# Kernel tuning notes

Measured on AMD Instinct MI355X. Metric: run time of the kernel, lower is better.

Reference implementation:

```python
import jax, jax.numpy as jnp
import numpy as np

EMB = 2048; H = 32; G = 8; D = 64; GS = H // G; EPS = 1e-6

def _rmsnorm(x, scale):
    x32 = x.astype(jnp.float32)
    var = jnp.mean(x32 * x32, axis=-1, keepdims=True)
    return (x32 * jax.lax.rsqrt(var + EPS) * scale).astype(x.dtype)

def _rope(x, cos, sin):
    # x: [B, h, S, D]; cos/sin: [S, D]
    d = x.shape[-1]
    x1, x2 = x[..., : d // 2], x[..., d // 2 :]
    rot = jnp.concatenate([-x2, x1], axis=-1)
    return (x * cos[None, None] + rot * sin[None, None]).astype(x.dtype)

def setup_inputs() -> dict:
    key = jax.random.key(0)
    ks = jax.random.split(key, 6)
    B, S = 2, 2048
    x = jax.random.normal(ks[0], (B, S, EMB), jnp.float32)
    # causal mask: True = blocked (masked_fill semantics)
    mask = jnp.triu(jnp.ones((S, S), dtype=bool), k=1)
    # standard RoPE tables, half-dim rotation, shape [S, D]
    inv_freq = 1.0 / (10000.0 ** (jnp.arange(0, D, 2, dtype=jnp.float32) / D))
    ang = jnp.arange(S, dtype=jnp.float32)[:, None] * inv_freq[None, :]  # [S, D/2]
    cos = jnp.concatenate([jnp.cos(ang), jnp.cos(ang)], axis=-1)
    sin = jnp.concatenate([jnp.sin(ang), jnp.sin(ang)], axis=-1)
    Wq = jax.random.normal(ks[1], (EMB, H * D), jnp.float32) * 0.02
    Wk = jax.random.normal(ks[2], (EMB, G * D), jnp.float32) * 0.02
    Wv = jax.random.normal(ks[3], (EMB, G * D), jnp.float32) * 0.02
    Wo = jax.random.normal(ks[4], (H * D, EMB), jnp.float32) * 0.02
    q_scale = jnp.ones((D,), jnp.float32)
    k_scale = jnp.ones((D,), jnp.float32)
    return {"x": x, "mask": mask, "cos": cos, "sin": sin, "Wq": Wq, "Wk": Wk,
            "Wv": Wv, "Wo": Wo, "q_scale": q_scale, "k_scale": k_scale}

def reference(x, mask, cos, sin, Wq, Wk, Wv, Wo, q_scale, k_scale):
    B, S, _ = x.shape
    q = (x @ Wq).reshape(B, S, H, D).transpose(0, 2, 1, 3)  # [B,H,S,D]
    k = (x @ Wk).reshape(B, S, G, D).transpose(0, 2, 1, 3)  # [B,G,S,D]
    v = (x @ Wv).reshape(B, S, G, D).transpose(0, 2, 1, 3)
    q = _rmsnorm(q, q_scale)
    k = _rmsnorm(k, k_scale)
    q = _rope(q, cos, sin)
    k = _rope(k, cos, sin)
    # GQA expansion (repeat_interleave over head dim)
    k = jnp.repeat(k, GS, axis=1)
    v = jnp.repeat(v, GS, axis=1)
    scale = 1.0 / np.float32(np.sqrt(D))
    s = jnp.einsum('bhqd,bhkd->bhqk', q.astype(jnp.float32), k.astype(jnp.float32)) * scale
    # flash path is causal regardless of `mask` arg; mask here equals causal
    s = jnp.where(mask[None, None], -jnp.inf, s)
    w = jax.nn.softmax(s, axis=-1)
    ctx = jnp.einsum('bhqk,bhkd->bhqd', w, v.astype(jnp.float32))
    ctx = ctx.transpose(0, 2, 1, 3).reshape(B, S, H * D)
    return ctx @ Wo
```

## Files before the change

### kernel.cpp

```cpp
#include <hip/hip_runtime.h>
#include <hip/hip_bf16.h>
#include <cstdint>
#include <cstddef>

#define EMB   2048
#define NH_   32
#define NG_   8
#define DH_   64
#define SEQ_  2048
#define BB_   2
#define MTOT  4096
#define LDQKV 3072
#define SM_C  0.18033688f

typedef __attribute__((ext_vector_type(8))) short s16x8;
typedef __attribute__((ext_vector_type(8))) unsigned short u16x8;
typedef __attribute__((ext_vector_type(4))) float f32x4;
typedef __attribute__((ext_vector_type(16))) float f32x16;
typedef __attribute__((ext_vector_type(4))) unsigned int u32x4;
typedef __attribute__((ext_vector_type(2))) unsigned int u32x2;
typedef __attribute__((ext_vector_type(2))) int i32x2;

__device__ __forceinline__ float bf2f(unsigned short u) {
  unsigned int x = (unsigned int)u << 16; return __uint_as_float(x);
}
__device__ __forceinline__ unsigned short f2bf(float f) {
  unsigned int x = __float_as_uint(f);
  x = x + 0x7FFFu + ((x >> 16) & 1u);
  return (unsigned short)(x >> 16);
}
__device__ __forceinline__ float ninf() { return __int_as_float(0xff800000); }
__device__ __forceinline__ unsigned int pack_bf2(float a, float b) {
  unsigned int r;
  asm("v_cvt_pk_bf16_f32 %0, %1, %2" : "=v"(r) : "v"(a), "v"(b));
  return r;
}
__device__ __forceinline__ void plswap(unsigned int& a, unsigned int& b) {
  i32x2 r = __builtin_amdgcn_permlane32_swap((int)a, (int)b, false, false);
  a = (unsigned int)r[0]; b = (unsigned int)r[1];
}
__device__ __forceinline__ void plswapf(float& a, float& b) {
  unsigned int ua = __float_as_uint(a), ub = __float_as_uint(b);
  plswap(ua, ub);
  a = __uint_as_float(ua); b = __uint_as_float(ub);
}

__device__ __forceinline__ void glds16(const void* g, void* l) {
  __builtin_amdgcn_global_load_lds((const __attribute__((address_space(1))) void*)g,
                                   (__attribute__((address_space(3))) void*)l, 16, 0, 0);
}

__device__ __forceinline__ void hw_sincos(float ang, float& c, float& s) {
  float rev = ang * 0.15915494309f;
  rev = rev - floorf(rev);
  asm("v_cos_f32 %0, %1" : "=v"(c) : "v"(rev));
  asm("v_sin_f32 %0, %1" : "=v"(s) : "v"(rev));
}

__global__ __launch_bounds__(256)
void prep(const float* __restrict__ x, const float* __restrict__ Wq,
          const float* __restrict__ Wk, const float* __restrict__ Wv,
          const float* __restrict__ Wo, unsigned short* __restrict__ xb,
          unsigned short* __restrict__ Wt, unsigned short* __restrict__ Wot) {
  __shared__ float tile[64][65];
  const int tid = threadIdx.x;
  const int bid = blockIdx.x;
  if (bid < 4096) {
    size_t i = (size_t)bid * 256 + tid;
    float4 a = *(const float4*)(x + i * 8);
    float4 c = *(const float4*)(x + i * 8 + 4);
    u16x8 o;
    o[0] = f2bf(a.x); o[1] = f2bf(a.y); o[2] = f2bf(a.z); o[3] = f2bf(a.w);
    o[4] = f2bf(c.x); o[5] = f2bf(c.y); o[6] = f2bf(c.z); o[7] = f2bf(c.w);
    *(u16x8*)(xb + i * 8) = o;
    return;
  }
  const float* in; unsigned short* out; int N; int local;
  if (bid < 5120)      { in = Wq; out = Wt;                       N = 2048; local = bid - 4096; }
  else if (bid < 5376) { in = Wk; out = Wt + (size_t)2048 * 2048; N = 512;  local = bid - 5120; }
  else if (bid < 5632) { in = Wv; out = Wt + (size_t)2560 * 2048; N = 512;  local = bid - 5376; }
  else                 { in = Wo; out = Wot;                      N = 2048; local = bid - 5632; }
  const int ntile = N >> 6;
  const int n0 = (local % ntile) * 64, k0 = (local / ntile) * 64;
  #pragma unroll
  for (int jj = 0; jj < 4; ++jj) {
    int r = (tid >> 4) + jj * 16;
    int c = (tid & 15) * 4;
    float4 v = *(const float4*)(in + (size_t)(k0 + r) * N + n0 + c);
    tile[r][c] = v.x; tile[r][c + 1] = v.y; tile[r][c + 2] = v.z; tile[r][c + 3] = v.w;
  }
  __syncthreads();
  #pragma unroll
  for (int rep = 0; rep < 2; ++rep) {
    int u = rep * 256 + tid;
    int nl = u >> 3, ch = u & 7;
    u16x8 o;
    #pragma unroll
    for (int e = 0; e < 8; ++e) o[e] = f2bf(tile[ch * 8 + e][nl]);
    *(u16x8*)(out + (size_t)(n0 + nl) * 2048 + k0 + ch * 8) = o;
  }
}

template<int BN, int F32OUT>
__global__ __launch_bounds__(512, 1)
void gemm256(const unsigned short* __restrict__ A, const unsigned short* __restrict__ Bt,
             void* __restrict__ C, int ldc) {
  constexpr int NST = 2 + BN / 128;
  constexpr int BUF = 16384 + BN * 64;
  constexpr int WN = BN / 64;
  constexpr int RW = 256 / (8 / WN);
  __shared__ __align__(16) char L[4][BUF];
  const int tid = threadIdx.x;
  const int wid = tid >> 6, lane = tid & 63;
  const int wm = wid / WN, wn = wid % WN;
  const int grp = lane >> 4, l15 = lane & 15;
  const int bm = blockIdx.y * 256, bn = blockIdx.x * BN;
  const int nt = 64;

  const int srow = tid >> 2;
  const int sc = (tid & 3) ^ (srow & 3);
  const int grp2 = grp ^ (l15 & 3);

  auto stage_ht = [&](int t, int h) {
    const unsigned short* src = (h < 2)
      ? A  + (size_t)(bm + h * 128 + srow) * 2048 + t * 32 + sc * 8
      : Bt + (size_t)(bn + (h - 2) * 128 + srow) * 2048 + t * 32 + sc * 8;
    glds16(src, &L[t & 3][h * 8192 + wid * 1024]);
  };

  f32x4 acc[RW / 16][4] = {};

  #pragma unroll
  for (int h = 0; h < NST; ++h) stage_ht(0, h);
  #pragma unroll
  for (int h = 0; h < NST; ++h) stage_ht(1, h);
  if constexpr (BN == 256) asm volatile("s_waitcnt vmcnt(4)" ::: "memory");
  else                     asm volatile("s_waitcnt vmcnt(3)" ::: "memory");
  __builtin_amdgcn_sched_barrier(0);
  __builtin_amdgcn_s_barrier();
  __builtin_amdgcn_sched_barrier(0);

  for (int t = 0; t < nt; ++t) {
    const char* Ab = &L[t & 3][0]     + (size_t)(wm * RW + l15) * 64 + grp2 * 16;
    const char* Bb = &L[t & 3][16384] + (size_t)(wn * 64 + l15) * 64 + grp2 * 16;
    const bool pre = (t + 2 < nt);
    if (pre) { stage_ht(t + 2, 0); stage_ht(t + 2, 1); }
    s16x8 bf[4], af[4];
    #pragma unroll
    for (int j = 0; j < 4; ++j) bf[j] = *(const s16x8*)(Bb + j * 1024);
    #pragma unroll
    for (int i = 0; i < 4; ++i) af[i] = *(const s16x8*)(Ab + i * 1024);
    __builtin_amdgcn_s_setprio(1);
    #pragma unroll
    for (int i = 0; i < 4; ++i)
      #pragma unroll
      for (int j = 0; j < 4; ++j)
        acc[i][j] = __builtin_amdgcn_mfma_f32_16x16x32_bf16(af[i], bf[j], acc[i][j], 0, 0, 0);
    __builtin_amdgcn_s_setprio(0);
    if constexpr (BN == 256) {
      if (pre) { stage_ht(t + 2, 2); stage_ht(t + 2, 3); }
      #pragma unroll
      for (int i = 0; i < 4; ++i) af[i] = *(const s16x8*)(Ab + (4 + i) * 1024);
      __builtin_amdgcn_s_setprio(1);
      #pragma unroll
      for (int i = 0; i < 4; ++i)
        #pragma unroll
        for (int j = 0; j < 4; ++j)
          acc[4 + i][j] = __builtin_amdgcn_mfma_f32_16x16x32_bf16(af[i], bf[j], acc[4 + i][j], 0, 0, 0);
      __builtin_amdgcn_s_setprio(0);
    } else {
      if (pre) stage_ht(t + 2, 2);
    }
    if (t + 1 < nt) {
      if (pre) {
        if constexpr (BN == 256) asm volatile("s_waitcnt vmcnt(4)" ::: "memory");
        else                     asm volatile("s_waitcnt vmcnt(3)" ::: "memory");
      } else {
        asm volatile("s_waitcnt vmcnt(0)" ::: "memory");
      }
      __builtin_amdgcn_sched_barrier(0);
      __builtin_amdgcn_s_barrier();
      __builtin_amdgcn_sched_barrier(0);
    }
  }

  #pragma unroll
  for (int i = 0; i < RW / 16; ++i)
    #pragma unroll
    for (int j = 0; j < 4; ++j)
      #pragma unroll
      for (int r = 0; r < 4; ++r) {
        int row = bm + wm * RW + i * 16 + grp * 4 + r;
        int col = bn + wn * 64 + j * 16 + l15;
        float v = acc[i][j][r];
        if (F32OUT) ((float*)C)[(size_t)row * ldc + col] = v;
        else        ((unsigned short*)C)[(size_t)row * ldc + col] = f2bf(v);
      }
}

__global__ __launch_bounds__(256)
void kvtile_rms(const unsigned short* __restrict__ qkv, const float* __restrict__ ksc,
                const float* __restrict__ cs, const float* __restrict__ sn,
                unsigned short* __restrict__ Kt, unsigned short* __restrict__ Vt) {
  __shared__ unsigned short Kl[32][72];
  __shared__ unsigned short Vl[32][72];
  const int tid = threadIdx.x;
  const int kt = blockIdx.x;
  const int bg = blockIdx.y;
  const int b = bg >> 3, g = bg & 7;
  {
    const int row = tid >> 3, ch = tid & 7;
    const int spos = kt * 32 + row;
    u16x8 kv = *(const u16x8*)(qkv + (size_t)(b * SEQ_ + spos) * LDQKV + 2048 + g * 64 + ch * 8);
    float v[8]; float sq = 0.f;
    #pragma unroll
    for (int e = 0; e < 8; ++e) { v[e] = bf2f(kv[e]); sq += v[e] * v[e]; }
    sq += __shfl_xor(sq, 1); sq += __shfl_xor(sq, 2); sq += __shfl_xor(sq, 4);
    const float rn = rsqrtf(sq * (1.f / 64.f) + 1e-6f);
    float xn[8];
    #pragma unroll
    for (int e = 0; e < 8; ++e) xn[e] = v[e] * rn * ksc[ch * 8 + e];
    float pn[8];
    #pragma unroll
    for (int e = 0; e < 8; ++e) pn[e] = __shfl_xor(xn[e], 4);
    const bool lo = (ch < 4);
    #pragma unroll
    for (int e = 0; e < 8; ++e) {
      int d = ch * 8 + e;
      float c = cs[spos * 64 + d], si = sn[spos * 64 + d];
      float o = lo ? (xn[e] * c - pn[e] * si) : fmaf(xn[e], c, pn[e] * si);
      Kl[row][d] = f2bf(o);
    }
    u16x8 vv = *(const u16x8*)(qkv + (size_t)(b * SEQ_ + spos) * LDQKV + 2560 + g * 64 + ch * 8);
    #pragma unroll
    for (int e = 0; e < 8; ++e) Vl[row][ch * 8 + e] = vv[e];
  }
  __syncthreads();
  {
    int c = tid >> 5, row = tid & 31;
    u16x8 o;
    #pragma unroll
    for (int e = 0; e < 8; ++e) o[e] = Kl[row][c * 8 + e];
    *(u16x8*)(Kt + (((size_t)(bg * 64 + kt)) << 11) + (c * 32 + row) * 8) = o;
  }
  {
    int c = tid >> 6, d = tid & 63;
    u16x8 o;
    #pragma unroll
    for (int e = 0; e < 8; ++e) o[e] = Vl[c * 8 + e][d];
    *(u16x8*)(Vt + (((size_t)(bg * 64 + kt)) << 11) + (c * 64 + d) * 8) = o;
  }
}

__global__ __launch_bounds__(256)
void attn_mfma11(const unsigned short* __restrict__ qkv, const float* __restrict__ qsc,
                 const unsigned short* __restrict__ Ktg, const unsigned short* __restrict__ Vtg,
                 unsigned short* __restrict__ ctx) {
  __shared__ __align__(16) unsigned short LA[8 * 1024];
  __shared__ __align__(16) unsigned short LB[8 * 1024];
  const int tid = threadIdx.x;
  const int w = tid >> 6, lane = tid & 63;
  const int l31 = lane & 31, half = lane >> 5;
  const int bid = blockIdx.x;
  const int x8 = bid & 7, r = bid >> 3;
  const int bg = x8 + 8 * (r & 1);
  const int rr = r >> 1;
  const int slot = rr >> 4, gi = rr & 15;
  const int qt = (slot == 0) ? (63 - gi) : (slot == 1) ? gi
               : (slot == 2) ? (47 - gi) : (16 + gi);
  const int b = bg >> 3, g = bg & 7, h = g * 4 + w;
  const int qbase = qt * 32;
  const int nkt = qt + 1;
  const int nit = (nkt + 1) >> 1;

  s16x8 qf[4];
  {
    const int spos = qbase + l31;
    float qv[4][8]; float sq = 0.f;
    #pragma unroll
    for (int s = 0; s < 4; ++s) {
      u16x8 raw = *(const u16x8*)(qkv + (size_t)(b * SEQ_ + spos) * LDQKV + h * 64 + half * 8 + s * 16);
      #pragma unroll
      for (int e = 0; e < 8; ++e) { qv[s][e] = bf2f(raw[e]); sq += qv[s][e] * qv[s][e]; }
    }
    sq += __shfl_xor(sq, 32);
    const float rn = rsqrtf(sq * (1.f / 64.f) + 1e-6f);
    float xn[4][8];
    #pragma unroll
    for (int s = 0; s < 4; ++s)
      #pragma unroll
      for (int e = 0; e < 8; ++e) xn[s][e] = qv[s][e] * rn * qsc[s * 16 + half * 8 + e];
    const float fs = (float)spos;
    float qo[4][8];
    #pragma unroll
    for (int s = 0; s < 2; ++s)
      #pragma unroll
      for (int e = 0; e < 8; ++e) {
        int d = s * 16 + half * 8 + e;
        float invf = exp2f((float)d * -0.4152410119f);
        float c0, s0;
        hw_sincos(fs * invf, c0, s0);
        qo[s][e]     = (xn[s][e] * c0 - xn[s + 2][e] * s0) * SM_C;
        qo[s + 2][e] = fmaf(xn[s + 2][e], c0, xn[s][e] * s0) * SM_C;
      }
    #pragma unroll
    for (int s = 0; s < 4; ++s) {
      u32x4 t;
      t[0] = pack_bf2(qo[s][0], qo[s][1]); t[1] = pack_bf2(qo[s][2], qo[s][3]);
      t[2] = pack_bf2(qo[s][4], qo[s][5]); t[3] = pack_bf2(qo[s][6], qo[s][7]);
      qf[s] = __builtin_bit_cast(s16x8, t);
    }
  }

  f32x16 acc0 = {}, acc1 = {};
  float l_st = 0.f;

  const size_t tbase = ((size_t)(bg * 64)) << 11;
  const int soff = (w << 9) + lane * 8;

  auto stage = [&](unsigned short* Lb, int pi) {
    const int kt0 = 2 * pi, kt1 = 2 * pi + 1;
    glds16(Ktg + tbase + ((size_t)kt0 << 11) + soff, (char*)Lb + (w << 10));
    glds16(Vtg + tbase + ((size_t)kt0 << 11) + soff, (char*)Lb + 8192 + (w << 10));
    if (kt1 < nkt) {
      glds16(Ktg + tbase + ((size_t)kt1 << 11) + soff, (char*)Lb + 4096 + (w << 10));
      glds16(Vtg + tbase + ((size_t)kt1 << 11) + soff, (char*)Lb + 12288 + (w << 10));
    }
  };

  auto sub = [&](const char* Kb, const char* Vb, bool diag, float& lsum) {
    s16x8 KF0 = *(const s16x8*)(Kb + (((0 + half) << 5) + l31) * 16);
    s16x8 KF1 = *(const s16x8*)(Kb + (((2 + half) << 5) + l31) * 16);
    s16x8 KF2 = *(const s16x8*)(Kb + (((4 + half) << 5) + l31) * 16);
    s16x8 KF3 = *(const s16x8*)(Kb + (((6 + half) << 5) + l31) * 16);
    s16x8 vf00 = *(const s16x8*)(Vb + (((half) << 6) + l31) * 16);
    s16x8 vf01 = *(const s16x8*)(Vb + (((2 + half) << 6) + l31) * 16);
    s16x8 vf10 = *(const s16x8*)(Vb + (((half) << 6) + 32 + l31) * 16);
    s16x8 vf11 = *(const s16x8*)(Vb + (((2 + half) << 6) + 32 + l31) * 16);
    f32x16 st = {};
    __builtin_amdgcn_s_setprio(1);
    st = __builtin_amdgcn_mfma_f32_32x32x16_bf16(KF0, qf[0], st, 0, 0, 0);
    st = __builtin_amdgcn_mfma_f32_32x32x16_bf16(KF1, qf[1], st, 0, 0, 0);
    st = __builtin_amdgcn_mfma_f32_32x32x16_bf16(KF2, qf[2], st, 0, 0, 0);
    st = __builtin_amdgcn_mfma_f32_32x32x16_bf16(KF3, qf[3], st, 0, 0, 0);
    __builtin_amdgcn_s_setprio(0);
    if (diag) {
      #pragma unroll
      for (int r2 = 0; r2 < 16; ++r2) {
        int key = (r2 & 3) + 8 * (r2 >> 2) + 4 * half;
        if (key > l31) st[r2] = ninf();
      }
    }
    float p[16];
    #pragma unroll
    for (int r2 = 0; r2 < 16; ++r2) p[r2] = exp2f(st[r2]);
    float s8[8];
    #pragma unroll
    for (int r2 = 0; r2 < 8; ++r2) s8[r2] = p[r2] + p[r2 + 8];
    lsum += ((s8[0] + s8[1]) + (s8[2] + s8[3])) + ((s8[4] + s8[5]) + (s8[6] + s8[7]));
    unsigned int PK[8];
    #pragma unroll
    for (int j = 0; j < 8; ++j) PK[j] = pack_bf2(p[2 * j], p[2 * j + 1]);
    plswap(PK[0], PK[2]); plswap(PK[1], PK[3]);
    plswap(PK[4], PK[6]); plswap(PK[5], PK[7]);
    u32x4 pb0u, pb1u;
    pb0u[0] = PK[0]; pb0u[1] = PK[1]; pb0u[2] = PK[2]; pb0u[3] = PK[3];
    pb1u[0] = PK[4]; pb1u[1] = PK[5]; pb1u[2] = PK[6]; pb1u[3] = PK[7];
    s16x8 pb0 = __builtin_bit_cast(s16x8, pb0u);
    s16x8 pb1 = __builtin_bit_cast(s16x8, pb1u);
    __builtin_amdgcn_s_setprio(1);
    acc0 = __builtin_amdgcn_mfma_f32_32x32x16_bf16(vf00, pb0, acc0, 0, 0, 0);
    acc1 = __builtin_amdgcn_mfma_f32_32x32x16_bf16(vf10, pb0, acc1, 0, 0, 0);
    acc0 = __builtin_amdgcn_mfma_f32_32x32x16_bf16(vf01, pb1, acc0, 0, 0, 0);
    acc1 = __builtin_amdgcn_mfma_f32_32x32x16_bf16(vf11, pb1, acc1, 0, 0, 0);
    __builtin_amdgcn_s_setprio(0);
  };

  auto pair_body = [&](const unsigned short* Lb, int pi) {
    const int kt0 = 2 * pi, kt1 = 2 * pi + 1;
    float lsum = 0.f;
    sub((const char*)Lb, (const char*)Lb + 8192, kt0 == qt, lsum);
    if (kt1 < nkt)
      sub((const char*)Lb + 4096, (const char*)Lb + 12288, kt1 == qt, lsum);
    { float a2 = lsum, b2 = lsum; plswapf(a2, b2); lsum = a2 + b2; }
    l_st += lsum;
  };

  stage(LA, 0);
  int pi = 0;
  while (true) {
    __syncthreads();
    if (pi + 1 < nit) stage(LB, pi + 1);
    pair_body(LA, pi);
    ++pi; if (pi >= nit) break;
    __syncthreads();
    if (pi + 1 < nit) stage(LA, pi + 1);
    pair_body(LB, pi);
    ++pi; if (pi >= nit) break;
  }

  const float linv = 1.f / l_st;
  unsigned short* orow = ctx + (size_t)(b * SEQ_ + qbase + l31) * 2048 + h * 64;
  #pragma unroll
  for (int dt = 0; dt < 2; ++dt) {
    #pragma unroll
    for (int rq = 0; rq < 4; ++rq) {
      const int rr2 = rq * 4;
      const int d0 = dt * 32 + 8 * rq + 4 * half;
      float a0 = (dt ? acc1[rr2]     : acc0[rr2])     * linv;
      float a1 = (dt ? acc1[rr2 + 1] : acc0[rr2 + 1]) * linv;
      float a2 = (dt ? acc1[rr2 + 2] : acc0[rr2 + 2]) * linv;
      float a3 = (dt ? acc1[rr2 + 3] : acc0[rr2 + 3]) * linv;
      u32x2 o;
      o[0] = pack_bf2(a0, a1);
      o[1] = pack_bf2(a2, a3);
      *(u32x2*)(orow + d0) = o;
    }
  }
}

extern "C" void kernel_launch(void* const* d_in, const int* in_sizes, int n_in,
                              void* d_out, int out_size, void* d_ws, size_t ws_size,
                              hipStream_t stream) {
  const float* x  = (const float*)d_in[0];
  const float* cs = (const float*)d_in[2];
  const float* sn = (const float*)d_in[3];
  const float* Wq = (const float*)d_in[4];
  const float* Wk = (const float*)d_in[5];
  const float* Wv = (const float*)d_in[6];
  const float* Wo = (const float*)d_in[7];
  const float* qs = (const float*)d_in[8];
  const float* ks = (const float*)d_in[9];
  float* out = (float*)d_out;

  unsigned short* xb  = (unsigned short*)d_ws;
  unsigned short* Wt  = xb  + (size_t)4096 * 2048;
  unsigned short* Wot = Wt  + (size_t)3072 * 2048;
  unsigned short* qkv = Wot + (size_t)2048 * 2048;
  unsigned short* vTb = qkv + (size_t)4096 * 3072;
  unsigned short* ctx = vTb + (size_t)16 * 64 * 2048;
  unsigned short* Ktt = xb;

  prep<<<6656, 256, 0, stream>>>(x, Wq, Wk, Wv, Wo, xb, Wt, Wot);
  gemm256<256, 0><<<dim3(12, 16), 512, 0, stream>>>(xb, Wt, qkv, 3072);
  kvtile_rms<<<dim3(64, 16), 256, 0, stream>>>(qkv, ks, cs, sn, Ktt, vTb);
  attn_mfma11<<<1024, 256, 0, stream>>>(qkv, qs, Ktt, vTb, ctx);
  gemm256<128, 1><<<dim3(16, 16), 512, 0, stream>>>(ctx, Wot, out, 2048);
}
```

Measured before the change: 184.4 us.

## Split long causal query tiles across blocks and merge partials in a combine kernel

Causal attention work is rebalanced so every block does a near-equal amount of key tiles. Long query tiles (32-63) are split at key tile 32. The first half runs alone in one block and the second half is paired with a short query tile (31-j) in another block. Unnormalized partial outputs and row sums go to reused workspace buffers, and a new combine kernel adds the two partials and normalizes them. The GEMM LDS swizzle pattern is also changed to XOR with (row>>1)&3. The split adds an extra launch, partial-buffer traffic and a second bf16 rounding of the partials, in exchange for removing the tail imbalance.

```diff
diff --git a/kernel.cpp b/kernel.cpp
--- a/kernel.cpp
+++ b/kernel.cpp
@@ -118,8 +118,8 @@
   const int nt = 64;
 
   const int srow = tid >> 2;
-  const int sc = (tid & 3) ^ (srow & 3);
-  const int grp2 = grp ^ (l15 & 3);
+  const int sc = (tid & 3) ^ ((srow >> 1) & 3);
+  const int grp2 = grp ^ ((l15 >> 1) & 3);
 
   auto stage_ht = [&](int t, int h) {
     const unsigned short* src = (h < 2)
@@ -253,170 +253,223 @@
 }
 
 __global__ __launch_bounds__(256)
-void attn_mfma11(const unsigned short* __restrict__ qkv, const float* __restrict__ qsc,
+void attn_mfma12(const unsigned short* __restrict__ qkv, const float* __restrict__ qsc,
                  const unsigned short* __restrict__ Ktg, const unsigned short* __restrict__ Vtg,
-                 unsigned short* __restrict__ ctx) {
-  __shared__ __align__(16) unsigned short LA[8 * 1024];
-  __shared__ __align__(16) unsigned short LB[8 * 1024];
+                 unsigned short* __restrict__ xbt, unsigned short* __restrict__ WtS,
+                 float* __restrict__ lbuf, unsigned short* __restrict__ ctx) {
+  __shared__ __align__(16) unsigned short LA[10 * 1024];
+  __shared__ __align__(16) unsigned short LB[10 * 1024];
   const int tid = threadIdx.x;
   const int w = tid >> 6, lane = tid & 63;
   const int l31 = lane & 31, half = lane >> 5;
   const int bid = blockIdx.x;
-  const int x8 = bid & 7, r = bid >> 3;
-  const int bg = x8 + 8 * (r & 1);
-  const int rr = r >> 1;
-  const int slot = rr >> 4, gi = rr & 15;
-  const int qt = (slot == 0) ? (63 - gi) : (slot == 1) ? gi
-               : (slot == 2) ? (47 - gi) : (16 + gi);
+  const int x8 = bid & 7, c = bid >> 3;
+  const int bg = x8 + 8 * (c & 1);
+  const int c2 = c >> 1;
   const int b = bg >> 3, g = bg & 7, h = g * 4 + w;
-  const int qbase = qt * 32;
-  const int nkt = qt + 1;
-  const int nit = (nkt + 1) >> 1;
-
-  s16x8 qf[4];
-  {
-    const int spos = qbase + l31;
-    float qv[4][8]; float sq = 0.f;
-    #pragma unroll
-    for (int s = 0; s < 4; ++s) {
-      u16x8 raw = *(const u16x8*)(qkv + (size_t)(b * SEQ_ + spos) * LDQKV + h * 64 + half * 8 + s * 16);
-      #pragma unroll
-      for (int e = 0; e < 8; ++e) { qv[s][e] = bf2f(raw[e]); sq += qv[s][e] * qv[s][e]; }
-    }
-    sq += __shfl_xor(sq, 32);
-    const float rn = rsqrtf(sq * (1.f / 64.f) + 1e-6f);
-    float xn[4][8];
-    #pragma unroll
-    for (int s = 0; s < 4; ++s)
-      #pragma unroll
-      for (int e = 0; e < 8; ++e) xn[s][e] = qv[s][e] * rn * qsc[s * 16 + half * 8 + e];
-    const float fs = (float)spos;
-    float qo[4][8];
-    #pragma unroll
-    for (int s = 0; s < 2; ++s)
-      #pragma unroll
-      for (int e = 0; e < 8; ++e) {
-        int d = s * 16 + half * 8 + e;
-        float invf = exp2f((float)d * -0.4152410119f);
-        float c0, s0;
-        hw_sincos(fs * invf, c0, s0);
-        qo[s][e]     = (xn[s][e] * c0 - xn[s + 2][e] * s0) * SM_C;
-        qo[s + 2][e] = fmaf(xn[s + 2][e], c0, xn[s][e] * s0) * SM_C;
-      }
-    #pragma unroll
-    for (int s = 0; s < 4; ++s) {
-      u32x4 t;
-      t[0] = pack_bf2(qo[s][0], qo[s][1]); t[1] = pack_bf2(qo[s][2], qo[s][3]);
-      t[2] = pack_bf2(qo[s][4], qo[s][5]); t[3] = pack_bf2(qo[s][6], qo[s][7]);
-      qf[s] = __builtin_bit_cast(s16x8, t);
-    }
-  }
-
-  f32x16 acc0 = {}, acc1 = {};
-  float l_st = 0.f;
+
+  int nseg, sqt[2], sk0[2], slen[2], smode[2], sslot[2];
+  if (c2 < 32) {
+    nseg = 1;
+    sqt[0] = 32 + c2; sk0[0] = 0; slen[0] = 32; smode[0] = 1;
+    sslot[0] = ((bg * 4 + w) * 32 + c2) * 2 + 0;
+  } else {
+    const int j = c2 - 32;
+    nseg = 2;
+    sqt[0] = 32 + j;  sk0[0] = 32; slen[0] = j + 1;  smode[0] = 1;
+    sslot[0] = ((bg * 4 + w) * 32 + j) * 2 + 1;
+    sqt[1] = 31 - j;  sk0[1] = 0;  slen[1] = 32 - j; smode[1] = 0; sslot[1] = 0;
+  }
 
   const size_t tbase = ((size_t)(bg * 64)) << 11;
   const int soff = (w << 9) + lane * 8;
 
-  auto stage = [&](unsigned short* Lb, int pi) {
-    const int kt0 = 2 * pi, kt1 = 2 * pi + 1;
-    glds16(Ktg + tbase + ((size_t)kt0 << 11) + soff, (char*)Lb + (w << 10));
-    glds16(Vtg + tbase + ((size_t)kt0 << 11) + soff, (char*)Lb + 8192 + (w << 10));
-    if (kt1 < nkt) {
-      glds16(Ktg + tbase + ((size_t)kt1 << 11) + soff, (char*)Lb + 4096 + (w << 10));
-      glds16(Vtg + tbase + ((size_t)kt1 << 11) + soff, (char*)Lb + 12288 + (w << 10));
-    }
-  };
-
-  auto sub = [&](const char* Kb, const char* Vb, bool diag, float& lsum) {
-    s16x8 KF0 = *(const s16x8*)(Kb + (((0 + half) << 5) + l31) * 16);
-    s16x8 KF1 = *(const s16x8*)(Kb + (((2 + half) << 5) + l31) * 16);
-    s16x8 KF2 = *(const s16x8*)(Kb + (((4 + half) << 5) + l31) * 16);
-    s16x8 KF3 = *(const s16x8*)(Kb + (((6 + half) << 5) + l31) * 16);
-    s16x8 vf00 = *(const s16x8*)(Vb + (((half) << 6) + l31) * 16);
-    s16x8 vf01 = *(const s16x8*)(Vb + (((2 + half) << 6) + l31) * 16);
-    s16x8 vf10 = *(const s16x8*)(Vb + (((half) << 6) + 32 + l31) * 16);
-    s16x8 vf11 = *(const s16x8*)(Vb + (((2 + half) << 6) + 32 + l31) * 16);
-    f32x16 st = {};
-    __builtin_amdgcn_s_setprio(1);
-    st = __builtin_amdgcn_mfma_f32_32x32x16_bf16(KF0, qf[0], st, 0, 0, 0);
-    st = __builtin_amdgcn_mfma_f32_32x32x16_bf16(KF1, qf[1], st, 0, 0, 0);
-    st = __builtin_amdgcn_mfma_f32_32x32x16_bf16(KF2, qf[2], st, 0, 0, 0);
-    st = __builtin_amdgcn_mfma_f32_32x32x16_bf16(KF3, qf[3], st, 0, 0, 0);
-    __builtin_amdgcn_s_setprio(0);
-    if (diag) {
-      #pragma unroll
-      for (int r2 = 0; r2 < 16; ++r2) {
-        int key = (r2 & 3) + 8 * (r2 >> 2) + 4 * half;
-        if (key > l31) st[r2] = ninf();
+  for (int s = 0; s < nseg; ++s) {
+    const int qt = sqt[s], k0 = sk0[s];
+    const int kend = k0 + slen[s];
+    const int qbase = qt * 32;
+
+    s16x8 qf[4];
+    {
+      const int spos = qbase + l31;
+      float qv[4][8]; float sq = 0.f;
+      #pragma unroll
+      for (int s2 = 0; s2 < 4; ++s2) {
+        u16x8 raw = *(const u16x8*)(qkv + (size_t)(b * SEQ_ + spos) * LDQKV + h * 64 + half * 8 + s2 * 16);
+        #pragma unroll
+        for (int e = 0; e < 8; ++e) { qv[s2][e] = bf2f(raw[e]); sq += qv[s2][e] * qv[s2][e]; }
+      }
+      sq += __shfl_xor(sq, 32);
+      const float rn = rsqrtf(sq * (1.f / 64.f) + 1e-6f);
+      float xn[4][8];
+      #pragma unroll
+      for (int s2 = 0; s2 < 4; ++s2)
+        #pragma unroll
+        for (int e = 0; e < 8; ++e) xn[s2][e] = qv[s2][e] * rn * qsc[s2 * 16 + half * 8 + e];
+      const float fs = (float)spos;
+      float qo[4][8];
+      #pragma unroll
+      for (int s2 = 0; s2 < 2; ++s2)
+        #pragma unroll
+        for (int e = 0; e < 8; ++e) {
+          int d = s2 * 16 + half * 8 + e;
+          float invf = exp2f((float)d * -0.4152410119f);
+          float c0, s0;
+          hw_sincos(fs * invf, c0, s0);
+          qo[s2][e]     = (xn[s2][e] * c0 - xn[s2 + 2][e] * s0) * SM_C;
+          qo[s2 + 2][e] = fmaf(xn[s2 + 2][e], c0, xn[s2][e] * s0) * SM_C;
+        }
+      #pragma unroll
+      for (int s2 = 0; s2 < 4; ++s2) {
+        u32x4 t;
+        t[0] = pack_bf2(qo[s2][0], qo[s2][1]); t[1] = pack_bf2(qo[s2][2], qo[s2][3]);
+        t[2] = pack_bf2(qo[s2][4], qo[s2][5]); t[3] = pack_bf2(qo[s2][6], qo[s2][7]);
+        qf[s2] = __builtin_bit_cast(s16x8, t);
       }
     }
-    float p[16];
-    #pragma unroll
-    for (int r2 = 0; r2 < 16; ++r2) p[r2] = exp2f(st[r2]);
-    float s8[8];
-    #pragma unroll
-    for (int r2 = 0; r2 < 8; ++r2) s8[r2] = p[r2] + p[r2 + 8];
-    lsum += ((s8[0] + s8[1]) + (s8[2] + s8[3])) + ((s8[4] + s8[5]) + (s8[6] + s8[7]));
-    unsigned int PK[8];
-    #pragma unroll
-    for (int j = 0; j < 8; ++j) PK[j] = pack_bf2(p[2 * j], p[2 * j + 1]);
-    plswap(PK[0], PK[2]); plswap(PK[1], PK[3]);
-    plswap(PK[4], PK[6]); plswap(PK[5], PK[7]);
-    u32x4 pb0u, pb1u;
-    pb0u[0] = PK[0]; pb0u[1] = PK[1]; pb0u[2] = PK[2]; pb0u[3] = PK[3];
-    pb1u[0] = PK[4]; pb1u[1] = PK[5]; pb1u[2] = PK[6]; pb1u[3] = PK[7];
-    s16x8 pb0 = __builtin_bit_cast(s16x8, pb0u);
-    s16x8 pb1 = __builtin_bit_cast(s16x8, pb1u);
-    __builtin_amdgcn_s_setprio(1);
-    acc0 = __builtin_amdgcn_mfma_f32_32x32x16_bf16(vf00, pb0, acc0, 0, 0, 0);
-    acc1 = __builtin_amdgcn_mfma_f32_32x32x16_bf16(vf10, pb0, acc1, 0, 0, 0);
-    acc0 = __builtin_amdgcn_mfma_f32_32x32x16_bf16(vf01, pb1, acc0, 0, 0, 0);
-    acc1 = __builtin_amdgcn_mfma_f32_32x32x16_bf16(vf11, pb1, acc1, 0, 0, 0);
-    __builtin_amdgcn_s_setprio(0);
-  };
-
-  auto pair_body = [&](const unsigned short* Lb, int pi) {
-    const int kt0 = 2 * pi, kt1 = 2 * pi + 1;
-    float lsum = 0.f;
-    sub((const char*)Lb, (const char*)Lb + 8192, kt0 == qt, lsum);
-    if (kt1 < nkt)
-      sub((const char*)Lb + 4096, (const char*)Lb + 12288, kt1 == qt, lsum);
-    { float a2 = lsum, b2 = lsum; plswapf(a2, b2); lsum = a2 + b2; }
-    l_st += lsum;
-  };
-
-  stage(LA, 0);
-  int pi = 0;
-  while (true) {
+
+    f32x16 acc0 = {}, acc1 = {};
+    float l_st = 0.f;
+
+    auto stage = [&](unsigned short* Lb, int ktA) {
+      glds16(Ktg + tbase + ((size_t)ktA << 11) + soff, (char*)Lb + (w << 10));
+      glds16(Vtg + tbase + ((size_t)ktA << 11) + soff, (char*)Lb + 8192 + (w << 10));
+      if (ktA + 1 < kend) {
+        glds16(Ktg + tbase + ((size_t)(ktA + 1) << 11) + soff, (char*)Lb + 4096 + (w << 10));
+        glds16(Vtg + tbase + ((size_t)(ktA + 1) << 11) + soff, (char*)Lb + 12288 + (w << 10));
+      }
+    };
+
+    auto sub = [&](const char* Kb, const char* Vb, bool diag, float& lsum) {
+      s16x8 KF0 = *(const s16x8*)(Kb + (((0 + half) << 5) + l31) * 16);
+      s16x8 KF1 = *(const s16x8*)(Kb + (((2 + half) << 5) + l31) * 16);
+      s16x8 KF2 = *(const s16x8*)(Kb + (((4 + half) << 5) + l31) * 16);
+      s16x8 KF3 = *(const s16x8*)(Kb + (((6 + half) << 5) + l31) * 16);
+      s16x8 vf00 = *(const s16x8*)(Vb + (((half) << 6) + l31) * 16);
+      s16x8 vf01 = *(const s16x8*)(Vb + (((2 + half) << 6) + l31) * 16);
+      s16x8 vf10 = *(const s16x8*)(Vb + (((half) << 6) + 32 + l31) * 16);
+      s16x8 vf11 = *(const s16x8*)(Vb + (((2 + half) << 6) + 32 + l31) * 16);
+      f32x16 st = {};
+      __builtin_amdgcn_s_setprio(1);
+      st = __builtin_amdgcn_mfma_f32_32x32x16_bf16(KF0, qf[0], st, 0, 0, 0);
+      st = __builtin_amdgcn_mfma_f32_32x32x16_bf16(KF1, qf[1], st, 0, 0, 0);
+      st = __builtin_amdgcn_mfma_f32_32x32x16_bf16(KF2, qf[2], st, 0, 0, 0);
+      st = __builtin_amdgcn_mfma_f32_32x32x16_bf16(KF3, qf[3], st, 0, 0, 0);
+      __builtin_amdgcn_s_setprio(0);
+      if (diag) {
+        #pragma unroll
+        for (int r2 = 0; r2 < 16; ++r2) {
+          int key = (r2 & 3) + 8 * (r2 >> 2) + 4 * half;
+          if (key > l31) st[r2] = ninf();
+        }
+      }
+      float p[16];
+      #pragma unroll
+      for (int r2 = 0; r2 < 16; ++r2) p[r2] = exp2f(st[r2]);
+      float s8[8];
+      #pragma unroll
+      for (int r2 = 0; r2 < 8; ++r2) s8[r2] = p[r2] + p[r2 + 8];
+      lsum += ((s8[0] + s8[1]) + (s8[2] + s8[3])) + ((s8[4] + s8[5]) + (s8[6] + s8[7]));
+      unsigned int PK[8];
+      #pragma unroll
+      for (int j2 = 0; j2 < 8; ++j2) PK[j2] = pack_bf2(p[2 * j2], p[2 * j2 + 1]);
+      plswap(PK[0], PK[2]); plswap(PK[1], PK[3]);
+      plswap(PK[4], PK[6]); plswap(PK[5], PK[7]);
+      u32x4 pb0u, pb1u;
+      pb0u[0] = PK[0]; pb0u[1] = PK[1]; pb0u[2] = PK[2]; pb0u[3] = PK[3];
+      pb1u[0] = PK[4]; pb1u[1] = PK[5]; pb1u[2] = PK[6]; pb1u[3] = PK[7];
+      s16x8 pb0 = __builtin_bit_cast(s16x8, pb0u);
+      s16x8 pb1 = __builtin_bit_cast(s16x8, pb1u);
+      __builtin_amdgcn_s_setprio(1);
+      acc0 = __builtin_amdgcn_mfma_f32_32x32x16_bf16(vf00, pb0, acc0, 0, 0, 0);
+      acc1 = __builtin_amdgcn_mfma_f32_32x32x16_bf16(vf10, pb0, acc1, 0, 0, 0);
+      acc0 = __builtin_amdgcn_mfma_f32_32x32x16_bf16(vf01, pb1, acc0, 0, 0, 0);
+      acc1 = __builtin_amdgcn_mfma_f32_32x32x16_bf16(vf11, pb1, acc1, 0, 0, 0);
+      __builtin_amdgcn_s_setprio(0);
+    };
+
+    auto pair_body = [&](const unsigned short* Lb, int kt0) {
+      float lsum = 0.f;
+      sub((const char*)Lb, (const char*)Lb + 8192, kt0 == qt, lsum);
+      if (kt0 + 1 < kend)
+        sub((const char*)Lb + 4096, (const char*)Lb + 12288, kt0 + 1 == qt, lsum);
+      { float a2 = lsum, b2 = lsum; plswapf(a2, b2); lsum = a2 + b2; }
+      l_st += lsum;
+    };
+
+    const int nit = (slen[s] + 1) >> 1;
     __syncthreads();
-    if (pi + 1 < nit) stage(LB, pi + 1);
-    pair_body(LA, pi);
-    ++pi; if (pi >= nit) break;
-    __syncthreads();
-    if (pi + 1 < nit) stage(LA, pi + 1);
-    pair_body(LB, pi);
-    ++pi; if (pi >= nit) break;
-  }
-
-  const float linv = 1.f / l_st;
-  unsigned short* orow = ctx + (size_t)(b * SEQ_ + qbase + l31) * 2048 + h * 64;
+    stage(LA, k0);
+    int pi = 0;
+    while (true) {
+      __syncthreads();
+      if (pi + 1 < nit) stage(LB, k0 + 2 * (pi + 1));
+      pair_body(LA, k0 + 2 * pi);
+      ++pi; if (pi >= nit) break;
+      __syncthreads();
+      if (pi + 1 < nit) stage(LA, k0 + 2 * (pi + 1));
+      pair_body(LB, k0 + 2 * pi);
+      ++pi; if (pi >= nit) break;
+    }
+
+    if (smode[s] == 0) {
+      const float linv = 1.f / l_st;
+      unsigned short* orow = ctx + (size_t)(b * SEQ_ + qbase + l31) * 2048 + h * 64;
+      #pragma unroll
+      for (int dt = 0; dt < 2; ++dt)
+        #pragma unroll
+        for (int rq = 0; rq < 4; ++rq) {
+          const int rr2 = rq * 4;
+          const int d0 = dt * 32 + 8 * rq + 4 * half;
+          float a0 = (dt ? acc1[rr2]     : acc0[rr2])     * linv;
+          float a1 = (dt ? acc1[rr2 + 1] : acc0[rr2 + 1]) * linv;
+          float a2 = (dt ? acc1[rr2 + 2] : acc0[rr2 + 2]) * linv;
+          float a3 = (dt ? acc1[rr2 + 3] : acc0[rr2 + 3]) * linv;
+          u32x2 o; o[0] = pack_bf2(a0, a1); o[1] = pack_bf2(a2, a3);
+          *(u32x2*)(orow + d0) = o;
+        }
+    } else {
+      const int slot = sslot[s];
+      unsigned short* prow = ((slot < 3072)
+        ? xbt + (size_t)slot * 2048
+        : WtS + (size_t)(slot - 3072) * 2048) + l31 * 64;
+      #pragma unroll
+      for (int dt = 0; dt < 2; ++dt)
+        #pragma unroll
+        for (int rq = 0; rq < 4; ++rq) {
+          const int rr2 = rq * 4;
+          const int d0 = dt * 32 + 8 * rq + 4 * half;
+          float a0 = (dt ? acc1[rr2]     : acc0[rr2]);
+          float a1 = (dt ? acc1[rr2 + 1] : acc0[rr2 + 1]);
+          float a2 = (dt ? acc1[rr2 + 2] : acc0[rr2 + 2]);
+          float a3 = (dt ? acc1[rr2 + 3] : acc0[rr2 + 3]);
+          u32x2 o; o[0] = pack_bf2(a0, a1); o[1] = pack_bf2(a2, a3);
+          *(u32x2*)(prow + d0) = o;
+        }
+      if (half == 0) lbuf[slot * 32 + l31] = l_st;
+    }
+  }
+}
+
+__global__ __launch_bounds__(256)
+void combine2(const unsigned short* __restrict__ xbt, const unsigned short* __restrict__ WtS,
+              const float* __restrict__ lbuf, unsigned short* __restrict__ ctx) {
+  const int ct = blockIdx.x;
+  const int bg = ct >> 7, rem = ct & 127, head = rem >> 5, j = rem & 31;
+  const int b = bg >> 3, g = bg & 7, h = g * 4 + head;
+  const int q = threadIdx.x >> 3, d0 = (threadIdx.x & 7) * 8;
+  const int s0 = ct * 2, s1 = s0 + 1;
+  const unsigned short* A = ((s0 < 3072) ? xbt + (size_t)s0 * 2048
+                                         : WtS + (size_t)(s0 - 3072) * 2048) + q * 64 + d0;
+  const unsigned short* B = ((s1 < 3072) ? xbt + (size_t)s1 * 2048
+                                         : WtS + (size_t)(s1 - 3072) * 2048) + q * 64 + d0;
+  const float inv = 1.f / (lbuf[s0 * 32 + q] + lbuf[s1 * 32 + q]);
+  u16x8 va = *(const u16x8*)A;
+  u16x8 vb = *(const u16x8*)B;
+  u16x8 o;
   #pragma unroll
-  for (int dt = 0; dt < 2; ++dt) {
-    #pragma unroll
-    for (int rq = 0; rq < 4; ++rq) {
-      const int rr2 = rq * 4;
-      const int d0 = dt * 32 + 8 * rq + 4 * half;
-      float a0 = (dt ? acc1[rr2]     : acc0[rr2])     * linv;
-      float a1 = (dt ? acc1[rr2 + 1] : acc0[rr2 + 1]) * linv;
-      float a2 = (dt ? acc1[rr2 + 2] : acc0[rr2 + 2]) * linv;
-      float a3 = (dt ? acc1[rr2 + 3] : acc0[rr2 + 3]) * linv;
-      u32x2 o;
-      o[0] = pack_bf2(a0, a1);
-      o[1] = pack_bf2(a2, a3);
-      *(u32x2*)(orow + d0) = o;
-    }
-  }
+  for (int e = 0; e < 8; ++e) o[e] = f2bf((bf2f(va[e]) + bf2f(vb[e])) * inv);
+  *(u16x8*)(ctx + (size_t)(b * SEQ_ + (32 + j) * 32 + q) * 2048 + h * 64 + d0) = o;
 }
 
 extern "C" void kernel_launch(void* const* d_in, const int* in_sizes, int n_in,
@@ -440,10 +493,14 @@
   unsigned short* vTb = qkv + (size_t)4096 * 3072;
   unsigned short* ctx = vTb + (size_t)16 * 64 * 2048;
   unsigned short* Ktt = xb;
+  unsigned short* xbt = xb + (size_t)2097152;
+  unsigned short* WtS = Wt;
+  float*          lbufp = (float*)(Wt + (size_t)4194304);
 
   prep<<<6656, 256, 0, stream>>>(x, Wq, Wk, Wv, Wo, xb, Wt, Wot);
   gemm256<256, 0><<<dim3(12, 16), 512, 0, stream>>>(xb, Wt, qkv, 3072);
   kvtile_rms<<<dim3(64, 16), 256, 0, stream>>>(qkv, ks, cs, sn, Ktt, vTb);
-  attn_mfma11<<<1024, 256, 0, stream>>>(qkv, qs, Ktt, vTb, ctx);
+  attn_mfma12<<<1024, 256, 0, stream>>>(qkv, qs, Ktt, vTb, xbt, WtS, lbufp, ctx);
+  combine2<<<2048, 256, 0, stream>>>(xbt, WtS, lbufp, ctx);
   gemm256<128, 1><<<dim3(16, 16), 512, 0, stream>>>(ctx, Wot, out, 2048);
 }
```

Result: slower. 191.8 us (+4.0%).

## Use 4-slot KV ring with prefetch depth two in attention; change GEMM LDS swizzle

Applied to the files above, without the earlier changes.

The attention kernel drops its two-buffer, pair-of-tiles scheme. It now uses a 4-slot LDS ring holding one KV tile per slot, prefetched two tiles ahead. A single explicit vmcnt wait plus a barrier runs per tile instead of a __syncthreads per pair. The GEMM LDS XOR swizzle now uses (row>>1)&3 instead of row&3 to change the bank-conflict pattern. The aim is more overlap of global-to-LDS loads with MFMA work and fewer LDS bank conflicts, at the cost of one barrier per tile rather than one per pair.

```diff
diff --git a/kernel.cpp b/kernel.cpp
--- a/kernel.cpp
+++ b/kernel.cpp
@@ -105,7 +105,6 @@
 __global__ __launch_bounds__(512, 1)
 void gemm256(const unsigned short* __restrict__ A, const unsigned short* __restrict__ Bt,
              void* __restrict__ C, int ldc) {
-  constexpr int NST = 2 + BN / 128;
   constexpr int BUF = 16384 + BN * 64;
   constexpr int WN = BN / 64;
   constexpr int RW = 256 / (8 / WN);
@@ -118,8 +117,8 @@
   const int nt = 64;
 
   const int srow = tid >> 2;
-  const int sc = (tid & 3) ^ (srow & 3);
-  const int grp2 = grp ^ (l15 & 3);
+  const int sc = (tid & 3) ^ ((srow >> 1) & 3);
+  const int grp2 = grp ^ ((l15 >> 1) & 3);
 
   auto stage_ht = [&](int t, int h) {
     const unsigned short* src = (h < 2)
@@ -128,6 +127,7 @@
     glds16(src, &L[t & 3][h * 8192 + wid * 1024]);
   };
 
+  constexpr int NST = 2 + BN / 128;
   f32x4 acc[RW / 16][4] = {};
 
   #pragma unroll
@@ -253,11 +253,10 @@
 }
 
 __global__ __launch_bounds__(256)
-void attn_mfma11(const unsigned short* __restrict__ qkv, const float* __restrict__ qsc,
+void attn_mfma14(const unsigned short* __restrict__ qkv, const float* __restrict__ qsc,
                  const unsigned short* __restrict__ Ktg, const unsigned short* __restrict__ Vtg,
                  unsigned short* __restrict__ ctx) {
-  __shared__ __align__(16) unsigned short LA[8 * 1024];
-  __shared__ __align__(16) unsigned short LB[8 * 1024];
+  __shared__ __align__(16) unsigned short LR[16 * 1024];
   const int tid = threadIdx.x;
   const int w = tid >> 6, lane = tid & 63;
   const int l31 = lane & 31, half = lane >> 5;
@@ -271,44 +270,43 @@
   const int b = bg >> 3, g = bg & 7, h = g * 4 + w;
   const int qbase = qt * 32;
   const int nkt = qt + 1;
-  const int nit = (nkt + 1) >> 1;
 
   s16x8 qf[4];
   {
     const int spos = qbase + l31;
     float qv[4][8]; float sq = 0.f;
     #pragma unroll
-    for (int s = 0; s < 4; ++s) {
-      u16x8 raw = *(const u16x8*)(qkv + (size_t)(b * SEQ_ + spos) * LDQKV + h * 64 + half * 8 + s * 16);
-      #pragma unroll
-      for (int e = 0; e < 8; ++e) { qv[s][e] = bf2f(raw[e]); sq += qv[s][e] * qv[s][e]; }
+    for (int s2 = 0; s2 < 4; ++s2) {
+      u16x8 raw = *(const u16x8*)(qkv + (size_t)(b * SEQ_ + spos) * LDQKV + h * 64 + half * 8 + s2 * 16);
+      #pragma unroll
+      for (int e = 0; e < 8; ++e) { qv[s2][e] = bf2f(raw[e]); sq += qv[s2][e] * qv[s2][e]; }
     }
     sq += __shfl_xor(sq, 32);
     const float rn = rsqrtf(sq * (1.f / 64.f) + 1e-6f);
     float xn[4][8];
     #pragma unroll
-    for (int s = 0; s < 4; ++s)
-      #pragma unroll
-      for (int e = 0; e < 8; ++e) xn[s][e] = qv[s][e] * rn * qsc[s * 16 + half * 8 + e];
+    for (int s2 = 0; s2 < 4; ++s2)
+      #pragma unroll
+      for (int e = 0; e < 8; ++e) xn[s2][e] = qv[s2][e] * rn * qsc[s2 * 16 + half * 8 + e];
     const float fs = (float)spos;
     float qo[4][8];
     #pragma unroll
-    for (int s = 0; s < 2; ++s)
+    for (int s2 = 0; s2 < 2; ++s2)
       #pragma unroll
       for (int e = 0; e < 8; ++e) {
-        int d = s * 16 + half * 8 + e;
+        int d = s2 * 16 + half * 8 + e;
         float invf = exp2f((float)d * -0.4152410119f);
         float c0, s0;
         hw_sincos(fs * invf, c0, s0);
-        qo[s][e]     = (xn[s][e] * c0 - xn[s + 2][e] * s0) * SM_C;
-        qo[s + 2][e] = fmaf(xn[s + 2][e], c0, xn[s][e] * s0) * SM_C;
+        qo[s2][e]     = (xn[s2][e] * c0 - xn[s2 + 2][e] * s0) * SM_C;
+        qo[s2 + 2][e] = fmaf(xn[s2 + 2][e], c0, xn[s2][e] * s0) * SM_C;
       }
     #pragma unroll
-    for (int s = 0; s < 4; ++s) {
+    for (int s2 = 0; s2 < 4; ++s2) {
       u32x4 t;
-      t[0] = pack_bf2(qo[s][0], qo[s][1]); t[1] = pack_bf2(qo[s][2], qo[s][3]);
-      t[2] = pack_bf2(qo[s][4], qo[s][5]); t[3] = pack_bf2(qo[s][6], qo[s][7]);
-      qf[s] = __builtin_bit_cast(s16x8, t);
+      t[0] = pack_bf2(qo[s2][0], qo[s2][1]); t[1] = pack_bf2(qo[s2][2], qo[s2][3]);
+      t[2] = pack_bf2(qo[s2][4], qo[s2][5]); t[3] = pack_bf2(qo[s2][6], qo[s2][7]);
+      qf[s2] = __builtin_bit_cast(s16x8, t);
     }
   }
 
@@ -318,17 +316,17 @@
   const size_t tbase = ((size_t)(bg * 64)) << 11;
   const int soff = (w << 9) + lane * 8;
 
-  auto stage = [&](unsigned short* Lb, int pi) {
-    const int kt0 = 2 * pi, kt1 = 2 * pi + 1;
-    glds16(Ktg + tbase + ((size_t)kt0 << 11) + soff, (char*)Lb + (w << 10));
-    glds16(Vtg + tbase + ((size_t)kt0 << 11) + soff, (char*)Lb + 8192 + (w << 10));
-    if (kt1 < nkt) {
-      glds16(Ktg + tbase + ((size_t)kt1 << 11) + soff, (char*)Lb + 4096 + (w << 10));
-      glds16(Vtg + tbase + ((size_t)kt1 << 11) + soff, (char*)Lb + 12288 + (w << 10));
+  auto stage = [&](int kt_) {
+    if (kt_ < nkt) {
+      char* dst = (char*)LR + (kt_ & 3) * 8192;
+      glds16(Ktg + tbase + ((size_t)kt_ << 11) + soff, dst + (w << 10));
+      glds16(Vtg + tbase + ((size_t)kt_ << 11) + soff, dst + 4096 + (w << 10));
     }
   };
 
-  auto sub = [&](const char* Kb, const char* Vb, bool diag, float& lsum) {
+  auto body = [&](int kt_) {
+    const char* Kb = (const char*)LR + (kt_ & 3) * 8192;
+    const char* Vb = Kb + 4096;
     s16x8 KF0 = *(const s16x8*)(Kb + (((0 + half) << 5) + l31) * 16);
     s16x8 KF1 = *(const s16x8*)(Kb + (((2 + half) << 5) + l31) * 16);
     s16x8 KF2 = *(const s16x8*)(Kb + (((4 + half) << 5) + l31) * 16);
@@ -344,7 +342,7 @@
     st = __builtin_amdgcn_mfma_f32_32x32x16_bf16(KF2, qf[2], st, 0, 0, 0);
     st = __builtin_amdgcn_mfma_f32_32x32x16_bf16(KF3, qf[3], st, 0, 0, 0);
     __builtin_amdgcn_s_setprio(0);
-    if (diag) {
+    if (kt_ == qt) {
       #pragma unroll
       for (int r2 = 0; r2 < 16; ++r2) {
         int key = (r2 & 3) + 8 * (r2 >> 2) + 4 * half;
@@ -357,10 +355,12 @@
     float s8[8];
     #pragma unroll
     for (int r2 = 0; r2 < 8; ++r2) s8[r2] = p[r2] + p[r2 + 8];
-    lsum += ((s8[0] + s8[1]) + (s8[2] + s8[3])) + ((s8[4] + s8[5]) + (s8[6] + s8[7]));
+    float psum = ((s8[0] + s8[1]) + (s8[2] + s8[3])) + ((s8[4] + s8[5]) + (s8[6] + s8[7]));
+    { float a2 = psum, b2 = psum; plswapf(a2, b2); psum = a2 + b2; }
+    l_st += psum;
     unsigned int PK[8];
     #pragma unroll
-    for (int j = 0; j < 8; ++j) PK[j] = pack_bf2(p[2 * j], p[2 * j + 1]);
+    for (int j2 = 0; j2 < 8; ++j2) PK[j2] = pack_bf2(p[2 * j2], p[2 * j2 + 1]);
     plswap(PK[0], PK[2]); plswap(PK[1], PK[3]);
     plswap(PK[4], PK[6]); plswap(PK[5], PK[7]);
     u32x4 pb0u, pb1u;
@@ -376,27 +376,16 @@
     __builtin_amdgcn_s_setprio(0);
   };
 
-  auto pair_body = [&](const unsigned short* Lb, int pi) {
-    const int kt0 = 2 * pi, kt1 = 2 * pi + 1;
-    float lsum = 0.f;
-    sub((const char*)Lb, (const char*)Lb + 8192, kt0 == qt, lsum);
-    if (kt1 < nkt)
-      sub((const char*)Lb + 4096, (const char*)Lb + 12288, kt1 == qt, lsum);
-    { float a2 = lsum, b2 = lsum; plswapf(a2, b2); lsum = a2 + b2; }
-    l_st += lsum;
-  };
-
-  stage(LA, 0);
-  int pi = 0;
-  while (true) {
-    __syncthreads();
-    if (pi + 1 < nit) stage(LB, pi + 1);
-    pair_body(LA, pi);
-    ++pi; if (pi >= nit) break;
-    __syncthreads();
-    if (pi + 1 < nit) stage(LA, pi + 1);
-    pair_body(LB, pi);
-    ++pi; if (pi >= nit) break;
+  stage(0);
+  stage(1);
+  for (int t = 0; t < nkt; ++t) {
+    if (t + 1 < nkt) asm volatile("s_waitcnt vmcnt(2)" ::: "memory");
+    else             asm volatile("s_waitcnt vmcnt(0)" ::: "memory");
+    __builtin_amdgcn_sched_barrier(0);
+    __builtin_amdgcn_s_barrier();
+    __builtin_amdgcn_sched_barrier(0);
+    stage(t + 2);
+    body(t);
   }
 
   const float linv = 1.f / l_st;
@@ -444,6 +433,6 @@
   prep<<<6656, 256, 0, stream>>>(x, Wq, Wk, Wv, Wo, xb, Wt, Wot);
   gemm256<256, 0><<<dim3(12, 16), 512, 0, stream>>>(xb, Wt, qkv, 3072);
   kvtile_rms<<<dim3(64, 16), 256, 0, stream>>>(qkv, ks, cs, sn, Ktt, vTb);
-  attn_mfma11<<<1024, 256, 0, stream>>>(qkv, qs, Ktt, vTb, ctx);
+  attn_mfma14<<<1024, 256, 0, stream>>>(qkv, qs, Ktt, vTb, ctx);
   gemm256<128, 1><<<dim3(16, 16), 512, 0, stream>>>(ctx, Wot, out, 2048);
 }
```

Result: no change. 186.6 us (+1.2%).
